# Kernel optimization log

Measured on AMD Instinct MI355X. Metric: run time of the kernel, lower is better.

## Reference

```python
import jax, jax.numpy as jnp
import numpy as np

C64 = jnp.complex64
INV_SQRT2 = 1.0 / np.sqrt(2.0)
_H = jnp.array([[INV_SQRT2, INV_SQRT2], [INV_SQRT2, -INV_SQRT2]], dtype=C64)
_CNOT = jnp.array([[1, 0, 0, 0], [0, 1, 0, 0], [0, 0, 0, 1], [0, 0, 1, 0]], dtype=C64)  # wire0=control (index = 2*b0 + b1)


def _rz(t):
    # diag(e^{-it/2}, e^{it/2})
    return jnp.diag(jnp.stack([jnp.exp(-0.5j * t), jnp.exp(0.5j * t)]))


def _ry(t):
    c, s = jnp.cos(0.5 * t), jnp.sin(0.5 * t)
    return jnp.stack([jnp.stack([c, -s]), jnp.stack([s, c])]).astype(C64)


def _phase(p):
    # diag(1, e^{ip})
    return jnp.diag(jnp.stack([jnp.ones((), C64), jnp.exp(1j * p)]))


def _layer_unitary(p):
    # p: [14] already clipped. Gate order: CNOT -> H x H -> PhaseShift -> Rot(r,0,phi_s)=RZ(r+phi_s)
    #   -> Rot(r,phi_d,0)=RY(phi_d)@RZ(r) -> CPhase(k0)*CPhase(k1) = diag(1,1,1,e^{i(k0+k1)}).
    # bs_theta (p[0]) and bs_phi (p[1]) are computed but never used in a gate, matching the source.
    P = jnp.kron(_phase(p[2]), _phase(p[3]))
    S = jnp.kron(_rz(p[4] + p[6]), _rz(p[5] + p[7]))
    D = jnp.kron(_ry(p[10]) @ _rz(p[8]), _ry(p[11]) @ _rz(p[9]))
    CP = jnp.diag(jnp.stack([jnp.ones((), C64), jnp.ones((), C64), jnp.ones((), C64),
                             jnp.exp(1j * (p[12] + p[13]))]))
    HH = jnp.kron(_H, _H)
    return CP @ D @ S @ P @ HH @ _CNOT


def _total_unitary(params):
    # params: [L, 14]. FraudLayerParameters.__post_init__ clips everything to +-5 (kerr to +-1).
    p = jnp.concatenate([jnp.clip(params[:, :12], -5.0, 5.0),
                         jnp.clip(params[:, 12:], -1.0, 1.0)], axis=1)
    U = jnp.eye(4, dtype=C64)
    for i in range(params.shape[0]):  # static, tiny layer count
        U = _layer_unitary(p[i]) @ U
    return U


def setup_inputs() -> dict:
    key = jax.random.key(0)
    k1, k2, k3, k4 = jax.random.split(key, 4)
    B, n_layers, n_classes = 4194304, 3, 1  # layer 0 = input layer, layers 1..2 = variational
    x = jax.random.normal(k1, (B, 2), dtype=jnp.float32)
    params = jax.random.uniform(k2, (n_layers, 14), dtype=jnp.float32, minval=-1.0, maxval=1.0)
    W = jax.random.normal(k3, (n_classes, 1), dtype=jnp.float32)
    b = jax.random.normal(k4, (n_classes,), dtype=jnp.float32)
    return {"x": x, "params": params, "W": W, "b": b}


def reference(x, params, W, b):
    U = _total_unitary(params)  # constant 4x4 (params don't depend on the sample)
    h = 0.5 * x
    c, s = jnp.cos(h), jnp.sin(h)
    # RX(t)|0> = [cos(t/2), -i sin(t/2)]
    a0 = jnp.stack([c[:, 0].astype(C64), (-1j) * s[:, 0].astype(C64)], axis=-1)  # [B,2]
    a1 = jnp.stack([c[:, 1].astype(C64), (-1j) * s[:, 1].astype(C64)], axis=-1)  # [B,2]
    state = (a0[:, :, None] * a1[:, None, :]).reshape(-1, 4)  # kron, index = 2*b0 + b1
    psi = state @ U.T  # [B,4] = einsum('ij,bj->bi')
    prob = jnp.real(psi * jnp.conj(psi))  # [B,4]
    z_sign = jnp.array([1.0, 1.0, -1.0, -1.0], dtype=jnp.float32)  # <Z on wire 0>
    logits = (prob @ z_sign)[:, None]  # [B,1]
    return logits @ W.T + b  # [B, n_classes]
```

## Files before the change

### kernel.cpp

```cpp
#include <hip/hip_runtime.h>
#include <math.h>


__device__ inline float eval_sample(float x0, float x1,
                                    float k00, float k01, float k02,
                                    float k10, float k11, float k12,
                                    float k20, float k21, float k22) {
    float s0, c0, s1, c1;
    __sincosf(x0, &s0, &c0);
    __sincosf(x1, &s1, &c1);
    float e0 = fmaf(s1, k02, fmaf(c1, k01, k00));
    float e1 = fmaf(s1, k12, fmaf(c1, k11, k10));
    float e2 = fmaf(s1, k22, fmaf(c1, k21, k20));
    return fmaf(s0, e2, fmaf(c0, e1, e0));
}

__global__ __launch_bounds__(256) void fraud_fused(
        const float* __restrict__ params, int n_layers,
        const float* __restrict__ W, const float* __restrict__ bias,
        const float4* __restrict__ x, float4* __restrict__ out, int nquads) {
    __shared__ float Am[16];

    const int t = threadIdx.x;
    const int gsize = gridDim.x * 256;
    const int q0 = blockIdx.x * 256 + t;
    const int q1 = q0 + gsize;
    const bool v0 = q0 < nquads, v1 = q1 < nquads;

    float4 xa0, xb0, xa1, xb1;
    if (v0) { xa0 = x[2 * q0]; xb0 = x[2 * q0 + 1]; }
    if (v1) { xa1 = x[2 * q1]; xb1 = x[2 * q1 + 1]; }
    const float w = W[0], bb = bias[0];

    if (t < 64) {
        const int i = (t >> 2) & 3, j = t & 3;
        const int i0 = i >> 1, i1 = i & 1;

        float Ur = (i == j) ? 1.f : 0.f, Ui = 0.f;

        for (int l = 0; l < n_layers; ++l) {
            float p[14];
            #pragma unroll
            for (int q = 0; q < 14; ++q) {
                float vv = params[l * 14 + q];
                float lim = (q < 12) ? 5.0f : 1.0f;
                p[q] = fminf(fmaxf(vv, -lim), lim);
            }
            float t0 = p[4] + p[6], t1 = p[5] + p[7];

            float sn8,  cs8;  __sincosf(0.5f * p[8],  &sn8,  &cs8);
            float sd10, cd10; __sincosf(0.5f * p[10], &sd10, &cd10);
            float sn9,  cs9;  __sincosf(0.5f * p[9],  &sn9,  &cs9);
            float sd11, cd11; __sincosf(0.5f * p[11], &sd11, &cd11);
            float mag00 = (i0 == 0) ?  cd10 : sd10;
            float mag01 = (i0 == 0) ? -sd10 : cd10;
            float d00r = mag00 * cs8, d00i = -mag00 * sn8;
            float d01r = mag01 * cs8, d01i =  mag01 * sn8;
            float mag10 = (i1 == 0) ?  cd11 : sd11;
            float mag11 = (i1 == 0) ? -sd11 : cd11;
            float e10r = mag10 * cs9, e10i = -mag10 * sn9;
            float e11r = mag11 * cs9, e11i =  mag11 * sn9;

            int sj = j ^ (j >> 1);
            float Lr = 0.f, Li = 0.f;
            #pragma unroll
            for (int k = 0; k < 4; ++k) {
                int k0 = k >> 1, k1 = k & 1;
                float ar = k0 ? d01r : d00r, ai = k0 ? d01i : d00i;
                float br = k1 ? e11r : e10r, bi = k1 ? e11i : e10i;
                float Dr = ar * br - ai * bi;
                float Di = ar * bi + ai * br;
                float th = p[2] * (float)k0 + p[3] * (float)k1
                         + 0.5f * t0 * (float)(2 * k0 - 1)
                         + 0.5f * t1 * (float)(2 * k1 - 1);
                float sth, cth; __sincosf(th, &sth, &cth);
                float hh = (__popc(k & sj) & 1) ? -0.5f : 0.5f;
                float Er2 = hh * cth, Ei2 = hh * sth;
                Lr += Dr * Er2 - Di * Ei2;
                Li += Dr * Ei2 + Di * Er2;
            }
            if (i == 3) {
                float cps, cpc; __sincosf(p[12] + p[13], &cps, &cpc);
                float nr = Lr * cpc - Li * cps;
                float ni = Lr * cps + Li * cpc;
                Lr = nr; Li = ni;
            }

            if (l == 0) { Ur = Lr; Ui = Li; }
            else {
                float nr = 0.f, ni = 0.f;
                #pragma unroll
                for (int k = 0; k < 4; ++k) {
                    float ar = __shfl(Lr, 4 * i + k, 64);
                    float ai = __shfl(Li, 4 * i + k, 64);
                    float br = __shfl(Ur, 4 * k + j, 64);
                    float bi = __shfl(Ui, 4 * k + j, 64);
                    nr = fmaf(ar, br, fmaf(-ai, bi, nr));
                    ni = fmaf(ar, bi, fmaf(ai, br, ni));
                }
                Ur = nr; Ui = ni;
            }
        }

        float mr = 0.f, mi = 0.f;
        #pragma unroll
        for (int k = 0; k < 4; ++k) {
            float z = (k < 2) ? 1.f : -1.f;
            float u1r =  __shfl(Ur, 4 * k + i, 64);
            float u1i = -__shfl(Ui, 4 * k + i, 64);
            float u2r =  __shfl(Ur, 4 * k + j, 64);
            float u2i =  __shfl(Ui, 4 * k + j, 64);
            mr += z * (u1r * u2r - u1i * u2i);
            mi += z * (u1r * u2i + u1i * u2r);
        }
        float dri = (i == 0) ? 1.f : ((i == 3) ? -1.f : 0.f);
        float dii = (i == 0 || i == 3) ? 0.f : -1.f;
        float drj = (j == 0) ? 1.f : ((j == 3) ? -1.f : 0.f);
        float dij = (j == 0 || j == 3) ? 0.f : -1.f;
        float fr = dri * drj + dii * dij;
        float fi = dri * dij - dii * drj;
        if (t < 16) Am[t] = mr * fr - mi * fi;
    }
    __syncthreads();

    float A00 = Am[0],  A01 = Am[1],  A02 = Am[2],  A03 = Am[3];
    float A11 = Am[5],  A12 = Am[6],  A13 = Am[7];
    float A22 = Am[10], A23 = Am[11], A33 = Am[15];
    float k00 = 0.25f * (A00 + A11 + A22 + A33) * w + bb;
    float k01 = 0.25f * (A00 - A11 + A22 - A33) * w;
    float k02 = 0.5f  * (A01 + A23) * w;
    float k10 = 0.25f * (A00 + A11 - A22 - A33) * w;
    float k11 = 0.25f * (A00 - A11 - A22 + A33) * w;
    float k12 = 0.5f  * (A01 - A23) * w;
    float k20 = 0.5f  * (A02 + A13) * w;
    float k21 = 0.5f  * (A02 - A13) * w;
    float k22 = 0.5f  * (A03 + A12) * w;

    if (v0) {
        float4 o;
        o.x = eval_sample(xa0.x, xa0.y, k00, k01, k02, k10, k11, k12, k20, k21, k22);
        o.y = eval_sample(xa0.z, xa0.w, k00, k01, k02, k10, k11, k12, k20, k21, k22);
        o.z = eval_sample(xb0.x, xb0.y, k00, k01, k02, k10, k11, k12, k20, k21, k22);
        o.w = eval_sample(xb0.z, xb0.w, k00, k01, k02, k10, k11, k12, k20, k21, k22);
        out[q0] = o;
    }
    if (v1) {
        float4 o;
        o.x = eval_sample(xa1.x, xa1.y, k00, k01, k02, k10, k11, k12, k20, k21, k22);
        o.y = eval_sample(xa1.z, xa1.w, k00, k01, k02, k10, k11, k12, k20, k21, k22);
        o.z = eval_sample(xb1.x, xb1.y, k00, k01, k02, k10, k11, k12, k20, k21, k22);
        o.w = eval_sample(xb1.z, xb1.w, k00, k01, k02, k10, k11, k12, k20, k21, k22);
        out[q1] = o;
    }
    for (int q = q1 + gsize; q < nquads; q += gsize) {
        float4 xa = x[2 * q];
        float4 xb = x[2 * q + 1];
        float4 o;
        o.x = eval_sample(xa.x, xa.y, k00, k01, k02, k10, k11, k12, k20, k21, k22);
        o.y = eval_sample(xa.z, xa.w, k00, k01, k02, k10, k11, k12, k20, k21, k22);
        o.z = eval_sample(xb.x, xb.y, k00, k01, k02, k10, k11, k12, k20, k21, k22);
        o.w = eval_sample(xb.z, xb.w, k00, k01, k02, k10, k11, k12, k20, k21, k22);
        out[q] = o;
    }
}

extern "C" void kernel_launch(void* const* d_in, const int* in_sizes, int n_in,
                              void* d_out, int out_size, void* d_ws, size_t ws_size,
                              hipStream_t stream) {
    const float* x      = (const float*)d_in[0];
    const float* params = (const float*)d_in[1];
    const float* W      = (const float*)d_in[2];
    const float* b      = (const float*)d_in[3];
    float* out = (float*)d_out;

    int n_layers = in_sizes[1] / 14;
    int B = out_size;
    int nq = B / 4;

    int blocks = (nq + 511) / 512;
    if (blocks > 2048) blocks = 2048;

    fraud_fused<<<blocks, 256, 0, stream>>>(params, n_layers, W, b,
                                            (const float4*)x, (float4*)out, nq);
}
```

Baseline: 15.19 us.

## Compute unitary per wavefront with shuffles, drop shared memory and grid-stride loop

Every wavefront now builds the 4x4 unitary and the per-sample coefficients itself and passes them between lanes with shuffles, so the shared-memory staging and the block-wide barrier go away. Work mapping changes to one float4 of input (two samples) and one float2 of output per item, with four items per thread spaced 64 apart within the wavefront. The launch covers the whole batch in one pass with no block cap and no grid-stride loop. In exchange the small unitary computation runs four times per block instead of once, and output stores are float2 rather than float4.

Measured after the change: 19.06 us. 1.26x slower.

```diff
diff --git a/kernel.cpp b/kernel.cpp
--- a/kernel.cpp
+++ b/kernel.cpp
@@ -2,130 +2,137 @@
 #include <math.h>
 
 
-__device__ inline float eval_sample(float x0, float x1,
-                                    float k00, float k01, float k02,
-                                    float k10, float k11, float k12,
-                                    float k20, float k21, float k22) {
+__device__ inline float2 eval_f4(float4 X,
+                                 float k00, float k01, float k02,
+                                 float k10, float k11, float k12,
+                                 float k20, float k21, float k22) {
     float s0, c0, s1, c1;
-    __sincosf(x0, &s0, &c0);
-    __sincosf(x1, &s1, &c1);
-    float e0 = fmaf(s1, k02, fmaf(c1, k01, k00));
-    float e1 = fmaf(s1, k12, fmaf(c1, k11, k10));
-    float e2 = fmaf(s1, k22, fmaf(c1, k21, k20));
-    return fmaf(s0, e2, fmaf(c0, e1, e0));
+    float2 r;
+    __sincosf(X.x, &s0, &c0);
+    __sincosf(X.y, &s1, &c1);
+    r.x = fmaf(s0, fmaf(s1, k22, fmaf(c1, k21, k20)),
+          fmaf(c0, fmaf(s1, k12, fmaf(c1, k11, k10)),
+                   fmaf(s1, k02, fmaf(c1, k01, k00))));
+    __sincosf(X.z, &s0, &c0);
+    __sincosf(X.w, &s1, &c1);
+    r.y = fmaf(s0, fmaf(s1, k22, fmaf(c1, k21, k20)),
+          fmaf(c0, fmaf(s1, k12, fmaf(c1, k11, k10)),
+                   fmaf(s1, k02, fmaf(c1, k01, k00))));
+    return r;
 }
 
 __global__ __launch_bounds__(256) void fraud_fused(
         const float* __restrict__ params, int n_layers,
         const float* __restrict__ W, const float* __restrict__ bias,
-        const float4* __restrict__ x, float4* __restrict__ out, int nquads) {
-    __shared__ float Am[16];
+        const float4* __restrict__ x4, float2* __restrict__ out2, int n4) {
+    const int t = threadIdx.x;
+    const int lane = t & 63;
+    const int gw = (blockIdx.x * 256 + t) >> 6;
+    const int f4b = gw * 256 + lane;
 
-    const int t = threadIdx.x;
-    const int gsize = gridDim.x * 256;
-    const int q0 = blockIdx.x * 256 + t;
-    const int q1 = q0 + gsize;
-    const bool v0 = q0 < nquads, v1 = q1 < nquads;
-
-    float4 xa0, xb0, xa1, xb1;
-    if (v0) { xa0 = x[2 * q0]; xb0 = x[2 * q0 + 1]; }
-    if (v1) { xa1 = x[2 * q1]; xb1 = x[2 * q1 + 1]; }
+    float4 X0, X1, X2, X3;
+    const bool b0 = f4b < n4, b1 = f4b + 64 < n4,
+               b2 = f4b + 128 < n4, b3 = f4b + 192 < n4;
+    if (b0) X0 = x4[f4b];
+    if (b1) X1 = x4[f4b + 64];
+    if (b2) X2 = x4[f4b + 128];
+    if (b3) X3 = x4[f4b + 192];
     const float w = W[0], bb = bias[0];
 
-    if (t < 64) {
-        const int i = (t >> 2) & 3, j = t & 3;
-        const int i0 = i >> 1, i1 = i & 1;
+    const int i = (lane >> 2) & 3, j = lane & 3;
+    const int i0 = i >> 1, i1 = i & 1;
 
-        float Ur = (i == j) ? 1.f : 0.f, Ui = 0.f;
+    float Ur = (i == j) ? 1.f : 0.f, Ui = 0.f;
 
-        for (int l = 0; l < n_layers; ++l) {
-            float p[14];
-            #pragma unroll
-            for (int q = 0; q < 14; ++q) {
-                float vv = params[l * 14 + q];
-                float lim = (q < 12) ? 5.0f : 1.0f;
-                p[q] = fminf(fmaxf(vv, -lim), lim);
-            }
-            float t0 = p[4] + p[6], t1 = p[5] + p[7];
+    for (int l = 0; l < n_layers; ++l) {
+        float p[14];
+        #pragma unroll
+        for (int q = 0; q < 14; ++q) {
+            float vv = params[l * 14 + q];
+            float lim = (q < 12) ? 5.0f : 1.0f;
+            p[q] = fminf(fmaxf(vv, -lim), lim);
+        }
+        float t0 = p[4] + p[6], t1 = p[5] + p[7];
 
-            float sn8,  cs8;  __sincosf(0.5f * p[8],  &sn8,  &cs8);
-            float sd10, cd10; __sincosf(0.5f * p[10], &sd10, &cd10);
-            float sn9,  cs9;  __sincosf(0.5f * p[9],  &sn9,  &cs9);
-            float sd11, cd11; __sincosf(0.5f * p[11], &sd11, &cd11);
-            float mag00 = (i0 == 0) ?  cd10 : sd10;
-            float mag01 = (i0 == 0) ? -sd10 : cd10;
-            float d00r = mag00 * cs8, d00i = -mag00 * sn8;
-            float d01r = mag01 * cs8, d01i =  mag01 * sn8;
-            float mag10 = (i1 == 0) ?  cd11 : sd11;
-            float mag11 = (i1 == 0) ? -sd11 : cd11;
-            float e10r = mag10 * cs9, e10i = -mag10 * sn9;
-            float e11r = mag11 * cs9, e11i =  mag11 * sn9;
+        float sn8,  cs8;  __sincosf(0.5f * p[8],  &sn8,  &cs8);
+        float sd10, cd10; __sincosf(0.5f * p[10], &sd10, &cd10);
+        float sn9,  cs9;  __sincosf(0.5f * p[9],  &sn9,  &cs9);
+        float sd11, cd11; __sincosf(0.5f * p[11], &sd11, &cd11);
+        float mag00 = (i0 == 0) ?  cd10 : sd10;
+        float mag01 = (i0 == 0) ? -sd10 : cd10;
+        float d00r = mag00 * cs8, d00i = -mag00 * sn8;
+        float d01r = mag01 * cs8, d01i =  mag01 * sn8;
+        float mag10 = (i1 == 0) ?  cd11 : sd11;
+        float mag11 = (i1 == 0) ? -sd11 : cd11;
+        float e10r = mag10 * cs9, e10i = -mag10 * sn9;
+        float e11r = mag11 * cs9, e11i =  mag11 * sn9;
 
-            int sj = j ^ (j >> 1);
-            float Lr = 0.f, Li = 0.f;
+        int sj = j ^ (j >> 1);
+        float Lr = 0.f, Li = 0.f;
+        #pragma unroll
+        for (int k = 0; k < 4; ++k) {
+            int k0 = k >> 1, k1 = k & 1;
+            float ar = k0 ? d01r : d00r, ai = k0 ? d01i : d00i;
+            float br = k1 ? e11r : e10r, bi = k1 ? e11i : e10i;
+            float Dr = ar * br - ai * bi;
+            float Di = ar * bi + ai * br;
+            float th = p[2] * (float)k0 + p[3] * (float)k1
+                     + 0.5f * t0 * (float)(2 * k0 - 1)
+                     + 0.5f * t1 * (float)(2 * k1 - 1);
+            float sth, cth; __sincosf(th, &sth, &cth);
+            float hh = (__popc(k & sj) & 1) ? -0.5f : 0.5f;
+            float Er2 = hh * cth, Ei2 = hh * sth;
+            Lr += Dr * Er2 - Di * Ei2;
+            Li += Dr * Ei2 + Di * Er2;
+        }
+        if (i == 3) {
+            float cps, cpc; __sincosf(p[12] + p[13], &cps, &cpc);
+            float nr = Lr * cpc - Li * cps;
+            float ni = Lr * cps + Li * cpc;
+            Lr = nr; Li = ni;
+        }
+
+        if (l == 0) { Ur = Lr; Ui = Li; }
+        else {
+            float nr = 0.f, ni = 0.f;
             #pragma unroll
             for (int k = 0; k < 4; ++k) {
-                int k0 = k >> 1, k1 = k & 1;
-                float ar = k0 ? d01r : d00r, ai = k0 ? d01i : d00i;
-                float br = k1 ? e11r : e10r, bi = k1 ? e11i : e10i;
-                float Dr = ar * br - ai * bi;
-                float Di = ar * bi + ai * br;
-                float th = p[2] * (float)k0 + p[3] * (float)k1
-                         + 0.5f * t0 * (float)(2 * k0 - 1)
-                         + 0.5f * t1 * (float)(2 * k1 - 1);
-                float sth, cth; __sincosf(th, &sth, &cth);
-                float hh = (__popc(k & sj) & 1) ? -0.5f : 0.5f;
-                float Er2 = hh * cth, Ei2 = hh * sth;
-                Lr += Dr * Er2 - Di * Ei2;
-                Li += Dr * Ei2 + Di * Er2;
+                float ar = __shfl(Lr, 4 * i + k, 64);
+                float ai = __shfl(Li, 4 * i + k, 64);
+                float br = __shfl(Ur, 4 * k + j, 64);
+                float bi = __shfl(Ui, 4 * k + j, 64);
+                nr = fmaf(ar, br, fmaf(-ai, bi, nr));
+                ni = fmaf(ar, bi, fmaf(ai, br, ni));
             }
-            if (i == 3) {
-                float cps, cpc; __sincosf(p[12] + p[13], &cps, &cpc);
-                float nr = Lr * cpc - Li * cps;
-                float ni = Lr * cps + Li * cpc;
-                Lr = nr; Li = ni;
-            }
+            Ur = nr; Ui = ni;
+        }
+    }
 
-            if (l == 0) { Ur = Lr; Ui = Li; }
-            else {
-                float nr = 0.f, ni = 0.f;
-                #pragma unroll
-                for (int k = 0; k < 4; ++k) {
-                    float ar = __shfl(Lr, 4 * i + k, 64);
-                    float ai = __shfl(Li, 4 * i + k, 64);
-                    float br = __shfl(Ur, 4 * k + j, 64);
-                    float bi = __shfl(Ui, 4 * k + j, 64);
-                    nr = fmaf(ar, br, fmaf(-ai, bi, nr));
-                    ni = fmaf(ar, bi, fmaf(ai, br, ni));
-                }
-                Ur = nr; Ui = ni;
-            }
-        }
+    float mr = 0.f, mi = 0.f;
+    #pragma unroll
+    for (int k = 0; k < 4; ++k) {
+        float z = (k < 2) ? 1.f : -1.f;
+        float u1r =  __shfl(Ur, 4 * k + i, 64);
+        float u1i = -__shfl(Ui, 4 * k + i, 64);
+        float u2r =  __shfl(Ur, 4 * k + j, 64);
+        float u2i =  __shfl(Ui, 4 * k + j, 64);
+        mr += z * (u1r * u2r - u1i * u2i);
+        mi += z * (u1r * u2i + u1i * u2r);
+    }
+    float dri = (i == 0) ? 1.f : ((i == 3) ? -1.f : 0.f);
+    float dii = (i == 0 || i == 3) ? 0.f : -1.f;
+    float drj = (j == 0) ? 1.f : ((j == 3) ? -1.f : 0.f);
+    float dij = (j == 0 || j == 3) ? 0.f : -1.f;
+    float fr = dri * drj + dii * dij;
+    float fi = dri * dij - dii * drj;
+    float Aval = mr * fr - mi * fi;
 
-        float mr = 0.f, mi = 0.f;
-        #pragma unroll
-        for (int k = 0; k < 4; ++k) {
-            float z = (k < 2) ? 1.f : -1.f;
-            float u1r =  __shfl(Ur, 4 * k + i, 64);
-            float u1i = -__shfl(Ui, 4 * k + i, 64);
-            float u2r =  __shfl(Ur, 4 * k + j, 64);
-            float u2i =  __shfl(Ui, 4 * k + j, 64);
-            mr += z * (u1r * u2r - u1i * u2i);
-            mi += z * (u1r * u2i + u1i * u2r);
-        }
-        float dri = (i == 0) ? 1.f : ((i == 3) ? -1.f : 0.f);
-        float dii = (i == 0 || i == 3) ? 0.f : -1.f;
-        float drj = (j == 0) ? 1.f : ((j == 3) ? -1.f : 0.f);
-        float dij = (j == 0 || j == 3) ? 0.f : -1.f;
-        float fr = dri * drj + dii * dij;
-        float fi = dri * dij - dii * drj;
-        if (t < 16) Am[t] = mr * fr - mi * fi;
-    }
-    __syncthreads();
+    float A00 = __shfl(Aval, 0, 64),  A01 = __shfl(Aval, 1, 64);
+    float A02 = __shfl(Aval, 2, 64),  A03 = __shfl(Aval, 3, 64);
+    float A11 = __shfl(Aval, 5, 64),  A12 = __shfl(Aval, 6, 64);
+    float A13 = __shfl(Aval, 7, 64),  A22 = __shfl(Aval, 10, 64);
+    float A23 = __shfl(Aval, 11, 64), A33 = __shfl(Aval, 15, 64);
 
-    float A00 = Am[0],  A01 = Am[1],  A02 = Am[2],  A03 = Am[3];
-    float A11 = Am[5],  A12 = Am[6],  A13 = Am[7];
-    float A22 = Am[10], A23 = Am[11], A33 = Am[15];
     float k00 = 0.25f * (A00 + A11 + A22 + A33) * w + bb;
     float k01 = 0.25f * (A00 - A11 + A22 - A33) * w;
     float k02 = 0.5f  * (A01 + A23) * w;
@@ -136,32 +143,10 @@
     float k21 = 0.5f  * (A02 - A13) * w;
     float k22 = 0.5f  * (A03 + A12) * w;
 
-    if (v0) {
-        float4 o;
-        o.x = eval_sample(xa0.x, xa0.y, k00, k01, k02, k10, k11, k12, k20, k21, k22);
-        o.y = eval_sample(xa0.z, xa0.w, k00, k01, k02, k10, k11, k12, k20, k21, k22);
-        o.z = eval_sample(xb0.x, xb0.y, k00, k01, k02, k10, k11, k12, k20, k21, k22);
-        o.w = eval_sample(xb0.z, xb0.w, k00, k01, k02, k10, k11, k12, k20, k21, k22);
-        out[q0] = o;
-    }
-    if (v1) {
-        float4 o;
-        o.x = eval_sample(xa1.x, xa1.y, k00, k01, k02, k10, k11, k12, k20, k21, k22);
-        o.y = eval_sample(xa1.z, xa1.w, k00, k01, k02, k10, k11, k12, k20, k21, k22);
-        o.z = eval_sample(xb1.x, xb1.y, k00, k01, k02, k10, k11, k12, k20, k21, k22);
-        o.w = eval_sample(xb1.z, xb1.w, k00, k01, k02, k10, k11, k12, k20, k21, k22);
-        out[q1] = o;
-    }
-    for (int q = q1 + gsize; q < nquads; q += gsize) {
-        float4 xa = x[2 * q];
-        float4 xb = x[2 * q + 1];
-        float4 o;
-        o.x = eval_sample(xa.x, xa.y, k00, k01, k02, k10, k11, k12, k20, k21, k22);
-        o.y = eval_sample(xa.z, xa.w, k00, k01, k02, k10, k11, k12, k20, k21, k22);
-        o.z = eval_sample(xb.x, xb.y, k00, k01, k02, k10, k11, k12, k20, k21, k22);
-        o.w = eval_sample(xb.z, xb.w, k00, k01, k02, k10, k11, k12, k20, k21, k22);
-        out[q] = o;
-    }
+    if (b0) out2[f4b]       = eval_f4(X0, k00,k01,k02,k10,k11,k12,k20,k21,k22);
+    if (b1) out2[f4b + 64]  = eval_f4(X1, k00,k01,k02,k10,k11,k12,k20,k21,k22);
+    if (b2) out2[f4b + 128] = eval_f4(X2, k00,k01,k02,k10,k11,k12,k20,k21,k22);
+    if (b3) out2[f4b + 192] = eval_f4(X3, k00,k01,k02,k10,k11,k12,k20,k21,k22);
 }
 
 extern "C" void kernel_launch(void* const* d_in, const int* in_sizes, int n_in,
@@ -175,11 +160,10 @@
 
     int n_layers = in_sizes[1] / 14;
     int B = out_size;
-    int nq = B / 4;
+    int n4 = B / 2;
 
-    int blocks = (nq + 511) / 512;
-    if (blocks > 2048) blocks = 2048;
+    int blocks = (n4 + 1023) / 1024;
 
     fraud_fused<<<blocks, 256, 0, stream>>>(params, n_layers, W, b,
-                                            (const float4*)x, (float4*)out, nq);
+                                            (const float4*)x, (float2*)out, n4);
 }
```
